# Kernel optimization log

Measured on AMD Instinct MI355X. Metric: run time of the kernel, lower is better.

Reference implementation:

```python
import jax, jax.numpy as jnp
import numpy as np


def setup_inputs() -> dict:
    key = jax.random.key(0)
    k0, k1, k2, k3, k4, k5 = jax.random.split(key, 6)
    T, B, V, L, H = 128, 128, 128000, 2, 1024  # seq_length, beam_size, vocab, layers, hidden
    return {
        "logprobsf": jax.random.normal(k0, (B, V), dtype=jnp.float32),
        "beam_seq": jax.random.randint(k1, (T, B), 0, V, dtype=jnp.int32),
        "beam_seq_logprobs": jax.random.normal(k2, (T, B), dtype=jnp.float32),
        "beam_logprob_sum": jax.random.normal(k3, (B,), dtype=jnp.float32),
        "state_h": jax.random.normal(k4, (L, B, H), dtype=jnp.float32),
        "state_c": jax.random.normal(k5, (L, B, H), dtype=jnp.float32),
        "t": 64,
        "beam_size": 128,
    }


def reference(logprobsf, beam_seq, beam_seq_logprobs, beam_logprob_sum, state_h, state_c, t, beam_size):
    """Vectorized, faithful beam_step (incl. the -1000 EOS penalty applied each
    timestep in beam_search before the step). t and beam_size are static ints."""
    V = logprobsf.shape[1]
    lp = logprobsf.at[:, V - 1].add(-1000.0)  # suppress EOS column

    cols = min(beam_size, V)
    rows = beam_size if t >= 1 else 1  # at t==0 all beams are identical

    # torch.sort descending + take first `cols` columns == top_k per row
    ys, ix = jax.lax.top_k(lp[:rows], cols)  # [rows, cols]

    # candidate total logprob for every (q, c) pair; pick global top beam_size
    cand_p = beam_logprob_sum[:rows, None] + ys  # [rows, cols]
    top_p, flat = jax.lax.top_k(cand_p.reshape(-1), beam_size)
    q_sel = flat // cols  # source beam per new beam
    c_sel = flat % cols   # rank within source beam's top-k

    tok = ix[q_sel, c_sel]  # chosen token ids, [beam_size]
    loc = ys[q_sel, c_sel]  # chosen local logprobs, [beam_size]

    # reorder beam history by source beam, then append step t
    new_seq = beam_seq.at[:t].set(beam_seq[:t, q_sel]).at[t].set(tok)
    new_logps = beam_seq_logprobs.at[:t].set(beam_seq_logprobs[:t, q_sel]).at[t].set(loc)
    new_sum = top_p

    # gather recurrent state along the beam dimension
    new_h = state_h[:, q_sel]
    new_c = state_c[:, q_sel]
    return new_seq, new_logps, new_sum, new_h, new_c
```

## Files before the change

kernel.cpp:

```cpp
#include <hip/hip_runtime.h>
#include <stdint.h>


#define HIST_SIZE 4096
#define CAP2 4096
#define FINCAP 512

__device__ __forceinline__ unsigned f2key(float f) {
  unsigned u = __float_as_uint(f);
  return (u & 0x80000000u) ? ~u : (u | 0x80000000u);
}
__device__ __forceinline__ float key2f(unsigned k) {
  unsigned u = (k & 0x80000000u) ? (k & 0x7fffffffu) : ~k;
  return __uint_as_float(u);
}

extern "C" __global__ void __launch_bounds__(256)
k_hist(const float* __restrict__ logp, const float* __restrict__ bsum,
       const int* __restrict__ tptr, int V, int bs,
       unsigned* __restrict__ ghist) {
  __shared__ unsigned hist[HIST_SIZE];
  for (int i = threadIdx.x; i < HIST_SIZE; i += 256) hist[i] = 0;
  __syncthreads();
  int t = *tptr;
  int rows = (t >= 1) ? bs : 1;
  long long stride = (long long)gridDim.x * 256;
  long long gid = (long long)blockIdx.x * 256 + threadIdx.x;
  if ((V & 3) == 0) {
    int V4 = V >> 2;
    long long total4 = (long long)rows * V4;
    const float4* lp4 = (const float4*)logp;
    for (long long i = gid; i < total4; i += stride) {
      int b = (int)(i / V4);
      int v0 = (int)(i - (long long)b * V4) << 2;
      float4 f = lp4[i];
      float s = bsum[b];
      float x0 = f.x, x1 = f.y, x2 = f.z, x3 = f.w;
      if (v0 + 3 == V - 1) x3 -= 1000.0f;
      atomicAdd(&hist[f2key(s + x0) >> 20], 1u);
      atomicAdd(&hist[f2key(s + x1) >> 20], 1u);
      atomicAdd(&hist[f2key(s + x2) >> 20], 1u);
      atomicAdd(&hist[f2key(s + x3) >> 20], 1u);
    }
  } else {
    long long total = (long long)rows * V;
    for (long long i = gid; i < total; i += stride) {
      int b = (int)(i / V);
      int v = (int)(i - (long long)b * V);
      float x = logp[i];
      if (v == V - 1) x -= 1000.0f;
      atomicAdd(&hist[f2key(bsum[b] + x) >> 20], 1u);
    }
  }
  __syncthreads();
  for (int i = threadIdx.x; i < HIST_SIZE; i += 256) {
    unsigned c = hist[i];
    if (c) atomicAdd(&ghist[i], c);
  }
}

extern "C" __global__ void __launch_bounds__(256)
k_thresh(const unsigned* __restrict__ ghist, int K, int* __restrict__ tbin_out) {
  __shared__ unsigned h[HIST_SIZE];
  __shared__ unsigned seg[256];
  int tid = threadIdx.x;
  for (int i = tid; i < HIST_SIZE; i += 256) h[i] = ghist[i];
  __syncthreads();
  unsigned s = 0;
#pragma unroll
  for (int j = 0; j < HIST_SIZE / 256; ++j) s += h[tid * (HIST_SIZE / 256) + j];
  seg[tid] = s;
  __syncthreads();
  if (tid == 0) {
    unsigned acc = 0;
    int tbin = 0;
    bool found = false;
    for (int sg = 255; sg >= 0 && !found; --sg) {
      if (acc + seg[sg] >= (unsigned)K) {
        int lo = sg * (HIST_SIZE / 256);
        for (int bn = lo + HIST_SIZE / 256 - 1; bn >= lo; --bn) {
          if (acc + h[bn] >= (unsigned)K) { tbin = bn; found = true; break; }
          acc += h[bn];
        }
      } else {
        acc += seg[sg];
      }
    }
    *tbin_out = tbin;
  }
}

extern "C" __global__ void __launch_bounds__(256)
k_collect(const float* __restrict__ logp, const float* __restrict__ bsum,
          const int* __restrict__ tptr, int V, int bs,
          const int* __restrict__ tbin_p,
          unsigned long long* __restrict__ cand, int* __restrict__ cnt) {
  int t = *tptr;
  int rows = (t >= 1) ? bs : 1;
  int tbin = *tbin_p;
  long long stride = (long long)gridDim.x * 256;
  long long gid = (long long)blockIdx.x * 256 + threadIdx.x;
  if ((V & 3) == 0) {
    int V4 = V >> 2;
    long long total4 = (long long)rows * V4;
    const float4* lp4 = (const float4*)logp;
    for (long long i = gid; i < total4; i += stride) {
      int b = (int)(i / V4);
      int v0 = (int)(i - (long long)b * V4) << 2;
      float4 f = lp4[i];
      float s = bsum[b];
      float xs[4] = {f.x, f.y, f.z, f.w};
      if (v0 + 3 == V - 1) xs[3] -= 1000.0f;
#pragma unroll
      for (int j = 0; j < 4; ++j) {
        unsigned key = f2key(s + xs[j]);
        if ((int)(key >> 20) >= tbin) {
          int pos = atomicAdd(cnt, 1);
          if (pos < CAP2) {
            unsigned flat = (unsigned)b * (unsigned)V + (unsigned)(v0 + j);
            cand[pos] = ((unsigned long long)key << 32) | (0xFFFFFFFFu - flat);
          }
        }
      }
    }
  } else {
    long long total = (long long)rows * V;
    for (long long i = gid; i < total; i += stride) {
      int b = (int)(i / V);
      int v = (int)(i - (long long)b * V);
      float x = logp[i];
      if (v == V - 1) x -= 1000.0f;
      unsigned key = f2key(bsum[b] + x);
      if ((int)(key >> 20) >= tbin) {
        int pos = atomicAdd(cnt, 1);
        if (pos < CAP2) {
          unsigned flat = (unsigned)b * (unsigned)V + (unsigned)v;
          cand[pos] = ((unsigned long long)key << 32) | (0xFFFFFFFFu - flat);
        }
      }
    }
  }
}

extern "C" __global__ void __launch_bounds__(256)
k_select(const float* __restrict__ logp, const int* __restrict__ cntp,
         const unsigned long long* __restrict__ cand_g, int V, int K,
         const int* __restrict__ tbin_p,
         float* __restrict__ out_sum, int* __restrict__ qsel,
         int* __restrict__ tok, float* __restrict__ loc) {
  __shared__ unsigned hist2[HIST_SIZE];
  __shared__ unsigned seg[256];
  __shared__ unsigned long long fin[FINCAP];
  __shared__ int sh_cnt_hi, sh_nfin, sh_tbin2;
  int tid = threadIdx.x;
  int n = *cntp;
  if (n > CAP2) n = CAP2;
  int tbin = *tbin_p;
  for (int i = tid; i < HIST_SIZE; i += 256) hist2[i] = 0;
  if (tid == 0) { sh_cnt_hi = 0; sh_nfin = 0; sh_tbin2 = 0; }
  __syncthreads();
  for (int i = tid; i < n; i += 256) {
    unsigned key = (unsigned)(cand_g[i] >> 32);
    int bin = (int)(key >> 20);
    if (bin > tbin) atomicAdd(&sh_cnt_hi, 1);
    else atomicAdd(&hist2[(key >> 8) & 0xFFFu], 1u);
  }
  __syncthreads();
  int cnt_hi = sh_cnt_hi;
  unsigned s = 0;
#pragma unroll
  for (int j = 0; j < HIST_SIZE / 256; ++j) s += hist2[tid * (HIST_SIZE / 256) + j];
  seg[tid] = s;
  __syncthreads();
  if (tid == 0) {
    unsigned need = (unsigned)(K - cnt_hi);
    unsigned acc = 0;
    int tb2 = 0;
    bool found = false;
    for (int sg = 255; sg >= 0 && !found; --sg) {
      if (acc + seg[sg] >= need) {
        int lo = sg * (HIST_SIZE / 256);
        for (int bn = lo + HIST_SIZE / 256 - 1; bn >= lo; --bn) {
          if (acc + hist2[bn] >= need) { tb2 = bn; found = true; break; }
          acc += hist2[bn];
        }
      } else {
        acc += seg[sg];
      }
    }
    sh_tbin2 = tb2;
  }
  __syncthreads();
  int tbin2 = sh_tbin2;
  for (int i = tid; i < n; i += 256) {
    unsigned long long c = cand_g[i];
    unsigned key = (unsigned)(c >> 32);
    int bin = (int)(key >> 20);
    bool keep = (bin > tbin) || ((int)((key >> 8) & 0xFFFu) >= tbin2);
    if (keep) {
      int pos = atomicAdd(&sh_nfin, 1);
      if (pos < FINCAP) fin[pos] = c;
    }
  }
  __syncthreads();
  int nf = sh_nfin;
  if (nf > FINCAP) nf = FINCAP;
  int m = 2;
  while (m < nf) m <<= 1;
  for (int i = nf + tid; i < m; i += 256) fin[i] = 0ull;
  __syncthreads();
  for (int k2 = 2; k2 <= m; k2 <<= 1) {
    for (int j = k2 >> 1; j > 0; j >>= 1) {
      for (int i = tid; i < m; i += 256) {
        int l = i ^ j;
        if (l > i) {
          unsigned long long ai = fin[i], al = fin[l];
          bool desc = ((i & k2) == 0);
          if (desc ? (ai < al) : (ai > al)) { fin[i] = al; fin[l] = ai; }
        }
      }
      __syncthreads();
    }
  }
  if (tid < K) {
    unsigned long long c = fin[tid];
    unsigned key = (unsigned)(c >> 32);
    unsigned flat = 0xFFFFFFFFu - (unsigned)(c & 0xFFFFFFFFull);
    int b = (int)(flat / (unsigned)V);
    int v = (int)(flat - (unsigned)b * (unsigned)V);
    out_sum[tid] = key2f(key);
    qsel[tid] = b;
    tok[tid] = v;
    float x = logp[(size_t)b * V + v];
    if (v == V - 1) x -= 1000.0f;
    loc[tid] = x;
  }
}

extern "C" __global__ void __launch_bounds__(256)
k_scatter(const int* __restrict__ beam_seq, const float* __restrict__ beam_lp,
          const float4* __restrict__ h4, const float4* __restrict__ c4,
          const int* __restrict__ tptr, const int* __restrict__ qsel,
          const int* __restrict__ tok, const float* __restrict__ loc,
          int T, int B, int LBH4, int H4,
          float* __restrict__ out, float4* __restrict__ outh4,
          float4* __restrict__ outc4) {
  int t = *tptr;
  size_t n_seq = (size_t)T * B;
  size_t scalar_items = 2 * n_seq;
  size_t total = scalar_items + 2 * (size_t)LBH4;
  size_t stride = (size_t)gridDim.x * 256;
  for (size_t j = (size_t)blockIdx.x * 256 + threadIdx.x; j < total; j += stride) {
    if (j < n_seq) {
      int ss = (int)(j / B), b = (int)(j % B);
      int val;
      if (ss < t)       val = beam_seq[(size_t)ss * B + qsel[b]];
      else if (ss == t) val = tok[b];
      else              val = beam_seq[j];
      out[j] = (float)val;
    } else if (j < scalar_items) {
      size_t jj = j - n_seq;
      int ss = (int)(jj / B), b = (int)(jj % B);
      float v;
      if (ss < t)       v = beam_lp[(size_t)ss * B + qsel[b]];
      else if (ss == t) v = loc[b];
      else              v = beam_lp[jj];
      out[j] = v;
    } else {
      size_t jj = j - scalar_items;
      bool is_c = jj >= (size_t)LBH4;
      size_t k = is_c ? jj - (size_t)LBH4 : jj;
      int row = (int)(k / H4);
      int h = (int)(k - (size_t)row * H4);
      int b = row % B;
      size_t src = (size_t)(row - b + qsel[b]) * H4 + h;
      if (is_c) outc4[k] = c4[src];
      else      outh4[k] = h4[src];
    }
  }
}

extern "C" void kernel_launch(void* const* d_in, const int* in_sizes, int n_in,
                              void* d_out, int out_size, void* d_ws, size_t ws_size,
                              hipStream_t stream) {
  const float* logp = (const float*)d_in[0];
  const int* beam_seq = (const int*)d_in[1];
  const float* beam_lp = (const float*)d_in[2];
  const float* bsum = (const float*)d_in[3];
  const float* st_h = (const float*)d_in[4];
  const float* st_c = (const float*)d_in[5];
  const int* tptr = (const int*)d_in[6];

  int B = in_sizes[3];
  int V = in_sizes[0] / B;
  int T = in_sizes[1] / B;
  int LBH = in_sizes[4];
  int LH = LBH / B;
  int bs = (out_size - 2 * in_sizes[1]) / (1 + 2 * LH);
  int H = 1024;
  int H4 = H / 4, LBH4 = LBH / 4;

  char* ws = (char*)d_ws;
  unsigned* ghist = (unsigned*)ws;
  int* cnt = (int*)(ws + 16384);
  int* tbin = (int*)(ws + 16388);
  unsigned long long* cand = (unsigned long long*)(ws + 16392);
  int* qsel = (int*)(ws + 16392 + CAP2 * 8);
  int* tok = qsel + bs;
  float* loc = (float*)(tok + bs);

  float* out = (float*)d_out;
  size_t n_seq = (size_t)T * B;
  float* out_sum = out + 2 * n_seq;
  float4* outh4 = (float4*)(out + 2 * n_seq + bs);
  float4* outc4 = outh4 + LBH4;

  hipMemsetAsync(d_ws, 0, 16392, stream);
  k_hist<<<1024, 256, 0, stream>>>(logp, bsum, tptr, V, bs, ghist);
  k_thresh<<<1, 256, 0, stream>>>(ghist, bs, tbin);
  k_collect<<<1024, 256, 0, stream>>>(logp, bsum, tptr, V, bs, tbin, cand, cnt);
  k_select<<<1, 256, 0, stream>>>(logp, cnt, cand, V, bs, tbin, out_sum, qsel, tok, loc);

  size_t total = 2 * n_seq + 2 * (size_t)LBH4;
  int blocks = (int)((total + 255) / 256);
  k_scatter<<<blocks, 256, 0, stream>>>(beam_seq, beam_lp,
                                        (const float4*)st_h, (const float4*)st_c,
                                        tptr, qsel, tok, loc,
                                        T, B, LBH4, H4, out, outh4, outc4);
}
```

Measured before the change: 163.7 us.

## Pick the top-k threshold from a sampled histogram and buffer candidates per block

```diff
diff --git a/kernel.cpp b/kernel.cpp
--- a/kernel.cpp
+++ b/kernel.cpp
@@ -2,9 +2,12 @@
 #include <stdint.h>
 
 
-#define HIST_SIZE 4096
-#define CAP2 4096
+#define SHIST 4096
+#define CAP 32768
+#define LCAP 256
 #define FINCAP 512
+
+typedef unsigned long long u64;
 
 __device__ __forceinline__ unsigned f2key(float f) {
   unsigned u = __float_as_uint(f);
@@ -15,196 +18,192 @@
   return __uint_as_float(u);
 }
 
-extern "C" __global__ void __launch_bounds__(256)
-k_hist(const float* __restrict__ logp, const float* __restrict__ bsum,
-       const int* __restrict__ tptr, int V, int bs,
-       unsigned* __restrict__ ghist) {
-  __shared__ unsigned hist[HIST_SIZE];
-  for (int i = threadIdx.x; i < HIST_SIZE; i += 256) hist[i] = 0;
+__device__ __forceinline__ void suffix_thresh(unsigned* h , unsigned* seg ,
+                                              unsigned target, int* sh_bin,
+                                              unsigned* sh_above, int tid) {
+  unsigned s = 0;
+#pragma unroll
+  for (int j = 0; j < SHIST / 256; ++j) s += h[tid * (SHIST / 256) + j];
+  seg[tid] = s;
+  __syncthreads();
+  for (int off = 1; off < 256; off <<= 1) {
+    unsigned add = (tid + off < 256) ? seg[tid + off] : 0;
+    __syncthreads();
+    seg[tid] += add;
+    __syncthreads();
+  }
+  unsigned excl = (tid + 1 < 256) ? seg[tid + 1] : 0;
+  unsigned incl = seg[tid];
+  if (tid == 0) { *sh_bin = 0; *sh_above = 0; }
+  __syncthreads();
+  if (excl < target && incl >= target) {
+    unsigned acc = excl;
+    int lo = tid * (SHIST / 256);
+    for (int bn = lo + SHIST / 256 - 1; bn >= lo; --bn) {
+      unsigned hb = h[bn];
+      if (acc + hb >= target) { *sh_bin = bn; *sh_above = acc; break; }
+      acc += hb;
+    }
+  }
+  __syncthreads();
+}
+
+extern "C" __global__ void __launch_bounds__(256)
+k_sample(const float* __restrict__ logp, const float* __restrict__ bsum,
+         const int* __restrict__ tptr, int V, int bs,
+         unsigned* __restrict__ shist) {
+  __shared__ unsigned hist[SHIST];
+  for (int i = threadIdx.x; i < SHIST; i += 256) hist[i] = 0;
   __syncthreads();
   int t = *tptr;
   int rows = (t >= 1) ? bs : 1;
-  long long stride = (long long)gridDim.x * 256;
-  long long gid = (long long)blockIdx.x * 256 + threadIdx.x;
-  if ((V & 3) == 0) {
-    int V4 = V >> 2;
-    long long total4 = (long long)rows * V4;
-    const float4* lp4 = (const float4*)logp;
-    for (long long i = gid; i < total4; i += stride) {
-      int b = (int)(i / V4);
-      int v0 = (int)(i - (long long)b * V4) << 2;
-      float4 f = lp4[i];
-      float s = bsum[b];
-      float x0 = f.x, x1 = f.y, x2 = f.z, x3 = f.w;
-      if (v0 + 3 == V - 1) x3 -= 1000.0f;
-      atomicAdd(&hist[f2key(s + x0) >> 20], 1u);
-      atomicAdd(&hist[f2key(s + x1) >> 20], 1u);
-      atomicAdd(&hist[f2key(s + x2) >> 20], 1u);
-      atomicAdd(&hist[f2key(s + x3) >> 20], 1u);
-    }
-  } else {
-    long long total = (long long)rows * V;
-    for (long long i = gid; i < total; i += stride) {
-      int b = (int)(i / V);
-      int v = (int)(i - (long long)b * V);
-      float x = logp[i];
+  long long total = (long long)rows * V;
+  long long step = total / gridDim.x;
+  long long start = (long long)blockIdx.x * step;
+  int tid = threadIdx.x;
+#pragma unroll 4
+  for (int j = 0; j < 16; ++j) {
+    long long idx = start + (long long)j * 256 + tid;
+    if (idx < total) {
+      int b = (int)(idx / V);
+      int v = (int)(idx - (long long)b * V);
+      float x = logp[idx];
       if (v == V - 1) x -= 1000.0f;
       atomicAdd(&hist[f2key(bsum[b] + x) >> 20], 1u);
     }
   }
   __syncthreads();
-  for (int i = threadIdx.x; i < HIST_SIZE; i += 256) {
+  for (int i = tid; i < SHIST; i += 256) {
     unsigned c = hist[i];
-    if (c) atomicAdd(&ghist[i], c);
-  }
-}
-
-extern "C" __global__ void __launch_bounds__(256)
-k_thresh(const unsigned* __restrict__ ghist, int K, int* __restrict__ tbin_out) {
-  __shared__ unsigned h[HIST_SIZE];
+    if (c) atomicAdd(&shist[i], c);
+  }
+}
+
+extern "C" __global__ void __launch_bounds__(256)
+k_pick(const unsigned* __restrict__ shist, int K, unsigned* __restrict__ tlo_key) {
+  __shared__ unsigned h[SHIST];
   __shared__ unsigned seg[256];
+  __shared__ int sh_bin;
+  __shared__ unsigned sh_above;
   int tid = threadIdx.x;
-  for (int i = tid; i < HIST_SIZE; i += 256) h[i] = ghist[i];
-  __syncthreads();
-  unsigned s = 0;
-#pragma unroll
-  for (int j = 0; j < HIST_SIZE / 256; ++j) s += h[tid * (HIST_SIZE / 256) + j];
-  seg[tid] = s;
-  __syncthreads();
-  if (tid == 0) {
-    unsigned acc = 0;
-    int tbin = 0;
-    bool found = false;
-    for (int sg = 255; sg >= 0 && !found; --sg) {
-      if (acc + seg[sg] >= (unsigned)K) {
-        int lo = sg * (HIST_SIZE / 256);
-        for (int bn = lo + HIST_SIZE / 256 - 1; bn >= lo; --bn) {
-          if (acc + h[bn] >= (unsigned)K) { tbin = bn; found = true; break; }
-          acc += h[bn];
-        }
-      } else {
-        acc += seg[sg];
-      }
-    }
-    *tbin_out = tbin;
-  }
-}
-
-extern "C" __global__ void __launch_bounds__(256)
-k_collect(const float* __restrict__ logp, const float* __restrict__ bsum,
-          const int* __restrict__ tptr, int V, int bs,
-          const int* __restrict__ tbin_p,
-          unsigned long long* __restrict__ cand, int* __restrict__ cnt) {
+  for (int i = tid; i < SHIST; i += 256) h[i] = shist[i];
+  __syncthreads();
+  suffix_thresh(h, seg, (unsigned)K, &sh_bin, &sh_above, tid);
+  if (tid == 0) *tlo_key = (unsigned)sh_bin << 20;
+}
+
+extern "C" __global__ void __launch_bounds__(256)
+k_main(const float* __restrict__ logp, const float* __restrict__ bsum,
+       const int* __restrict__ tptr, int V, int bs,
+       const unsigned* __restrict__ tlo_p,
+       u64* __restrict__ cand, int* __restrict__ cnt) {
+  __shared__ u64 lbuf[LCAP];
+  __shared__ int lcnt, lbase;
+  int tid = threadIdx.x;
+  if (tid == 0) lcnt = 0;
+  __syncthreads();
   int t = *tptr;
   int rows = (t >= 1) ? bs : 1;
-  int tbin = *tbin_p;
-  long long stride = (long long)gridDim.x * 256;
-  long long gid = (long long)blockIdx.x * 256 + threadIdx.x;
+  unsigned tlo = *tlo_p;
   if ((V & 3) == 0) {
-    int V4 = V >> 2;
-    long long total4 = (long long)rows * V4;
+    unsigned V4 = (unsigned)V >> 2;
+    unsigned total4 = (unsigned)rows * V4;
+    unsigned stride = gridDim.x * 256;
     const float4* lp4 = (const float4*)logp;
-    for (long long i = gid; i < total4; i += stride) {
-      int b = (int)(i / V4);
-      int v0 = (int)(i - (long long)b * V4) << 2;
+    for (unsigned i = blockIdx.x * 256 + tid; i < total4; i += stride) {
+      unsigned b = i / V4;
+      unsigned v0 = (i - b * V4) << 2;
       float4 f = lp4[i];
       float s = bsum[b];
       float xs[4] = {f.x, f.y, f.z, f.w};
-      if (v0 + 3 == V - 1) xs[3] -= 1000.0f;
+      if (v0 + 3 == (unsigned)V - 1) xs[3] -= 1000.0f;
 #pragma unroll
       for (int j = 0; j < 4; ++j) {
         unsigned key = f2key(s + xs[j]);
-        if ((int)(key >> 20) >= tbin) {
-          int pos = atomicAdd(cnt, 1);
-          if (pos < CAP2) {
-            unsigned flat = (unsigned)b * (unsigned)V + (unsigned)(v0 + j);
-            cand[pos] = ((unsigned long long)key << 32) | (0xFFFFFFFFu - flat);
+        if (key >= tlo) {
+          int p = atomicAdd(&lcnt, 1);
+          if (p < LCAP) {
+            unsigned flat = b * (unsigned)V + v0 + j;
+            lbuf[p] = ((u64)key << 32) | (0xFFFFFFFFu - flat);
           }
         }
       }
     }
   } else {
     long long total = (long long)rows * V;
-    for (long long i = gid; i < total; i += stride) {
+    long long stride = (long long)gridDim.x * 256;
+    for (long long i = (long long)blockIdx.x * 256 + tid; i < total; i += stride) {
       int b = (int)(i / V);
       int v = (int)(i - (long long)b * V);
       float x = logp[i];
       if (v == V - 1) x -= 1000.0f;
       unsigned key = f2key(bsum[b] + x);
-      if ((int)(key >> 20) >= tbin) {
-        int pos = atomicAdd(cnt, 1);
-        if (pos < CAP2) {
+      if (key >= tlo) {
+        int p = atomicAdd(&lcnt, 1);
+        if (p < LCAP) {
           unsigned flat = (unsigned)b * (unsigned)V + (unsigned)v;
-          cand[pos] = ((unsigned long long)key << 32) | (0xFFFFFFFFu - flat);
+          lbuf[p] = ((u64)key << 32) | (0xFFFFFFFFu - flat);
         }
       }
     }
   }
+  __syncthreads();
+  int n = lcnt < LCAP ? lcnt : LCAP;
+  if (tid == 0) lbase = atomicAdd(cnt, n);
+  __syncthreads();
+  int base = lbase;
+  for (int i = tid; i < n; i += 256) {
+    int g = base + i;
+    if (g < CAP) cand[g] = lbuf[i];
+  }
 }
 
 extern "C" __global__ void __launch_bounds__(256)
 k_select(const float* __restrict__ logp, const int* __restrict__ cntp,
-         const unsigned long long* __restrict__ cand_g, int V, int K,
-         const int* __restrict__ tbin_p,
+         const u64* __restrict__ cand_g, int V, int K,
          float* __restrict__ out_sum, int* __restrict__ qsel,
          int* __restrict__ tok, float* __restrict__ loc) {
-  __shared__ unsigned hist2[HIST_SIZE];
+  __shared__ unsigned hist[SHIST];
   __shared__ unsigned seg[256];
-  __shared__ unsigned long long fin[FINCAP];
-  __shared__ int sh_cnt_hi, sh_nfin, sh_tbin2;
+  __shared__ u64 fin[FINCAP];
+  __shared__ int sh_bin, sh_nfin;
+  __shared__ unsigned sh_above;
   int tid = threadIdx.x;
   int n = *cntp;
-  if (n > CAP2) n = CAP2;
-  int tbin = *tbin_p;
-  for (int i = tid; i < HIST_SIZE; i += 256) hist2[i] = 0;
-  if (tid == 0) { sh_cnt_hi = 0; sh_nfin = 0; sh_tbin2 = 0; }
+  if (n > CAP) n = CAP;
+  for (int i = tid; i < SHIST; i += 256) hist[i] = 0;
+  if (tid == 0) sh_nfin = 0;
+  __syncthreads();
+  for (int i = tid; i < n; i += 256)
+    atomicAdd(&hist[(unsigned)(cand_g[i] >> 52)], 1u);
+  __syncthreads();
+  suffix_thresh(hist, seg, (unsigned)K, &sh_bin, &sh_above, tid);
+  int tbin = sh_bin;
+  unsigned cnt_hi = sh_above;
+  __syncthreads();
+  for (int i = tid; i < SHIST; i += 256) hist[i] = 0;
   __syncthreads();
   for (int i = tid; i < n; i += 256) {
     unsigned key = (unsigned)(cand_g[i] >> 32);
-    int bin = (int)(key >> 20);
-    if (bin > tbin) atomicAdd(&sh_cnt_hi, 1);
-    else atomicAdd(&hist2[(key >> 8) & 0xFFFu], 1u);
-  }
-  __syncthreads();
-  int cnt_hi = sh_cnt_hi;
-  unsigned s = 0;
-#pragma unroll
-  for (int j = 0; j < HIST_SIZE / 256; ++j) s += hist2[tid * (HIST_SIZE / 256) + j];
-  seg[tid] = s;
-  __syncthreads();
-  if (tid == 0) {
-    unsigned need = (unsigned)(K - cnt_hi);
-    unsigned acc = 0;
-    int tb2 = 0;
-    bool found = false;
-    for (int sg = 255; sg >= 0 && !found; --sg) {
-      if (acc + seg[sg] >= need) {
-        int lo = sg * (HIST_SIZE / 256);
-        for (int bn = lo + HIST_SIZE / 256 - 1; bn >= lo; --bn) {
-          if (acc + hist2[bn] >= need) { tb2 = bn; found = true; break; }
-          acc += hist2[bn];
-        }
-      } else {
-        acc += seg[sg];
-      }
-    }
-    sh_tbin2 = tb2;
-  }
-  __syncthreads();
-  int tbin2 = sh_tbin2;
+    if ((int)(key >> 20) == tbin) atomicAdd(&hist[(key >> 8) & 0xFFFu], 1u);
+  }
+  __syncthreads();
+  unsigned need = (unsigned)K - cnt_hi;
+  suffix_thresh(hist, seg, need, &sh_bin, &sh_above, tid);
+  int tbin2 = sh_bin;
+  __syncthreads();
   for (int i = tid; i < n; i += 256) {
-    unsigned long long c = cand_g[i];
+    u64 c = cand_g[i];
     unsigned key = (unsigned)(c >> 32);
     int bin = (int)(key >> 20);
-    bool keep = (bin > tbin) || ((int)((key >> 8) & 0xFFFu) >= tbin2);
+    bool keep = (bin > tbin) || (bin == tbin && (int)((key >> 8) & 0xFFFu) >= tbin2);
     if (keep) {
-      int pos = atomicAdd(&sh_nfin, 1);
-      if (pos < FINCAP) fin[pos] = c;
-    }
-  }
-  __syncthreads();
-  int nf = sh_nfin;
-  if (nf > FINCAP) nf = FINCAP;
+      int p = atomicAdd(&sh_nfin, 1);
+      if (p < FINCAP) fin[p] = c;
+    }
+  }
+  __syncthreads();
+  int nf = sh_nfin < FINCAP ? sh_nfin : FINCAP;
   int m = 2;
   while (m < nf) m <<= 1;
   for (int i = nf + tid; i < m; i += 256) fin[i] = 0ull;
@@ -214,7 +213,7 @@
       for (int i = tid; i < m; i += 256) {
         int l = i ^ j;
         if (l > i) {
-          unsigned long long ai = fin[i], al = fin[l];
+          u64 ai = fin[i], al = fin[l];
           bool desc = ((i & k2) == 0);
           if (desc ? (ai < al) : (ai > al)) { fin[i] = al; fin[l] = ai; }
         }
@@ -223,7 +222,7 @@
     }
   }
   if (tid < K) {
-    unsigned long long c = fin[tid];
+    u64 c = fin[tid];
     unsigned key = (unsigned)(c >> 32);
     unsigned flat = 0xFFFFFFFFu - (unsigned)(c & 0xFFFFFFFFull);
     int b = (int)(flat / (unsigned)V);
@@ -301,11 +300,11 @@
   int H4 = H / 4, LBH4 = LBH / 4;
 
   char* ws = (char*)d_ws;
-  unsigned* ghist = (unsigned*)ws;
+  unsigned* shist = (unsigned*)ws;
   int* cnt = (int*)(ws + 16384);
-  int* tbin = (int*)(ws + 16388);
-  unsigned long long* cand = (unsigned long long*)(ws + 16392);
-  int* qsel = (int*)(ws + 16392 + CAP2 * 8);
+  unsigned* tlo_key = (unsigned*)(ws + 16388);
+  u64* cand = (u64*)(ws + 16392);
+  int* qsel = (int*)(ws + 16392 + CAP * 8);
   int* tok = qsel + bs;
   float* loc = (float*)(tok + bs);
 
@@ -316,10 +315,10 @@
   float4* outc4 = outh4 + LBH4;
 
   hipMemsetAsync(d_ws, 0, 16392, stream);
-  k_hist<<<1024, 256, 0, stream>>>(logp, bsum, tptr, V, bs, ghist);
-  k_thresh<<<1, 256, 0, stream>>>(ghist, bs, tbin);
-  k_collect<<<1024, 256, 0, stream>>>(logp, bsum, tptr, V, bs, tbin, cand, cnt);
-  k_select<<<1, 256, 0, stream>>>(logp, cnt, cand, V, bs, tbin, out_sum, qsel, tok, loc);
+  k_sample<<<256, 256, 0, stream>>>(logp, bsum, tptr, V, bs, shist);
+  k_pick<<<1, 256, 0, stream>>>(shist, bs, tlo_key);
+  k_main<<<1024, 256, 0, stream>>>(logp, bsum, tptr, V, bs, tlo_key, cand, cnt);
+  k_select<<<1, 256, 0, stream>>>(logp, cnt, cand, V, bs, out_sum, qsel, tok, loc);
 
   size_t total = 2 * n_seq + 2 * (size_t)LBH4;
   int blocks = (int)((total + 255) / 256);
```

After: 157.7 us. 1.04x faster.
